# Kernel tuning notes

Hardware: AMD Instinct MI355X
Metric: run time of the kernel (lower is better)

Reference implementation:

```python
import jax, jax.numpy as jnp
import numpy as np

B, N, F = 8, 1024, 256
OUT, REL = 256, 16
NADJ = 7  # ((2 relations + consecutive) * 2 for backward) + self link


def setup_inputs() -> dict:
    key = jax.random.key(0)
    k0, k1, k2, k3, k4 = jax.random.split(key, 5)
    features = jax.random.normal(k0, (B, N, F), dtype=jnp.float32)
    A1 = jax.random.uniform(k1, (B, N, N), dtype=jnp.float32)
    A2 = jax.random.uniform(k2, (B, N, N), dtype=jnp.float32)
    # learned params: one (F+REL, OUT) weight per adjacency matrix, edge embeddings init 'ones', bias (N, OUT)
    W = jax.random.normal(k3, (NADJ, F + REL, OUT), dtype=jnp.float32) * 0.05
    W_edges = jnp.ones((NADJ, REL), dtype=jnp.float32)
    b = jax.random.uniform(k4, (N, OUT), dtype=jnp.float32, minval=-0.05, maxval=0.05)
    return {"features": features, "A1": A1, "A2": A2, "W": W, "W_edges": W_edges, "b": b}


def reference(features, A1, A2, W, W_edges, b):
    # eye = A[0] * zeros(N) + eye(N)  -> batch-broadcast identity [B,N,N]
    eye = jnp.zeros_like(A1) + jnp.eye(N, dtype=A1.dtype)
    # original rolls along axis 0 (batch) of the broadcast identity (faithful replication)
    shifted = jnp.roll(eye, 1, axis=0)
    A_fwd = [A1, A2, shifted]                      # relations + consecutive link
    A_list = A_fwd + [jnp.swapaxes(a, 1, 2) for a in A_fwd]  # backward links
    A_list.append(eye)                             # self links
    A = jnp.stack(A_list, axis=0)                  # [R,B,N,N]

    # concat(features, tile(W_edges[r])) @ W[r] == features @ W[r][:F] + W_edges[r] @ W[r][F:]
    HW = jnp.einsum('bnf,rfo->rbno', features, W[:, :F]) \
         + jnp.einsum('rd,rdo->ro', W_edges, W[:, F:])[:, None, None, :]  # [R,B,N,OUT]
    AHW = jnp.einsum('rbnm,rbmo->rbno', A, HW)     # batched adjacency matmul
    out = jnp.max(AHW, axis=0) + b                 # max-aggregate over relations, add bias
    return out                                     # activation = linear
```

## Files before the change

### kernel.cpp

```cpp
#include <hip/hip_runtime.h>
#include <hip/hip_bf16.h>

#define B_ 8
#define N_ 1024
#define F_ 256
#define OUT_ 256
#define REL_ 16
#define NADJ_ 7

typedef __attribute__((ext_vector_type(8))) _Float16 f16x8;
typedef __attribute__((ext_vector_type(4))) float f32x4;

__device__ __forceinline__ void gll16(const _Float16* g, _Float16* l) {
    __builtin_amdgcn_global_load_lds(
        (const __attribute__((address_space(1))) void*)g,
        (__attribute__((address_space(3))) void*)l, 16, 0, 0);
}

__constant__ const int c_perm[7] = {0, 1, 3, 4, 2, 5, 6};

__global__ __launch_bounds__(256) void prep_kernel(const float* __restrict__ W,
                                                   const float* __restrict__ We,
                                                   const float* __restrict__ feat,
                                                   float* __restrict__ cb,
                                                   _Float16* __restrict__ WTp,
                                                   _Float16* __restrict__ Fe) {
    int bid = blockIdx.x, tid = threadIdx.x;
    if (bid < 7) {
        int idx = bid * 256 + tid;
        int j = idx / OUT_, o = idx % OUT_;
        int r = c_perm[j];
        const float* Wr = W + (size_t)r * (F_ + REL_) * OUT_;
        float s = 0.f;
#pragma unroll
        for (int d = 0; d < REL_; ++d) s += We[r * REL_ + d] * Wr[(F_ + d) * OUT_ + o];
        cb[idx] = s;
    } else if (bid < 1799) {
        int idx = (bid - 7) * 256 + tid;
        int j = idx >> 16, rem = idx & 65535, o = rem >> 8, f = rem & 255;
        int r = c_perm[j];
        WTp[idx] = (_Float16)W[((size_t)r * (F_ + REL_) + f) * OUT_ + o];
    } else {
        int i = (bid - 1799) * 256 + tid;
        size_t base = (size_t)i * 8;
        float4 a = *(const float4*)(feat + base);
        float4 b = *(const float4*)(feat + base + 4);
        f16x8 v = {(_Float16)a.x, (_Float16)a.y, (_Float16)a.z, (_Float16)a.w,
                   (_Float16)b.x, (_Float16)b.y, (_Float16)b.z, (_Float16)b.w};
        *(f16x8*)(Fe + base) = v;
    }
}

__global__ __launch_bounds__(256) void convhw_kernel(const float* __restrict__ A1,
                                                     const float* __restrict__ A2,
                                                     const _Float16* __restrict__ Fe,
                                                     const _Float16* __restrict__ WTp,
                                                     const float* __restrict__ cb,
                                                     _Float16* __restrict__ Af,
                                                     _Float16* __restrict__ HWT,
                                                     _Float16* __restrict__ HWN) {
    __shared__ _Float16 S[8192];
    const int bid = blockIdx.x, tid = threadIdx.x;
    if (bid < 896) {
        const int z = bid / 128, rem = bid % 128, bx = rem & 63, by = rem >> 6;
        const bool tr = (z < 4);
        const _Float16* A  = tr ? (WTp + (size_t)z * 65536) : Fe;
        const _Float16* Bt = tr ? Fe : (WTp + (size_t)z * 65536);
        const int m0 = (tr ? by : bx) * 128;
        const int n0 = (tr ? bx : by) * 128;
        _Float16* As = S;
        _Float16* Bs = S + 4096;
        const int wave = tid >> 6, lane = tid & 63, lm = lane & 15, q = lane >> 4;
        const int wr = (wave >> 1) * 64, wc = (wave & 1) * 64;
        const int srow = tid >> 2, sk = (tid & 3) * 8;
        const _Float16* ga0 = A + (size_t)(m0 + srow) * F_ + sk;
        const _Float16* ga1 = ga0 + (size_t)64 * F_;
        const _Float16* gb0 = Bt + (size_t)(n0 + srow) * F_ + sk;
        const _Float16* gb1 = gb0 + (size_t)64 * F_;
        _Float16* la0 = As + tid * 8;
        _Float16* la1 = As + 2048 + tid * 8;
        _Float16* lb0 = Bs + tid * 8;
        _Float16* lb1 = Bs + 2048 + tid * 8;

        f32x4 acc[4][4] = {};
        for (int k0 = 0; k0 < F_; k0 += 32) {
            gll16(ga0 + k0, la0);
            gll16(ga1 + k0, la1);
            gll16(gb0 + k0, lb0);
            gll16(gb1 + k0, lb1);
            __syncthreads();
            f16x8 af[4], bf[4];
#pragma unroll
            for (int i = 0; i < 4; ++i) af[i] = *(const f16x8*)(As + (wr + i * 16 + lm) * 32 + q * 8);
#pragma unroll
            for (int j = 0; j < 4; ++j) bf[j] = *(const f16x8*)(Bs + (wc + j * 16 + lm) * 32 + q * 8);
#pragma unroll
            for (int i = 0; i < 4; ++i)
#pragma unroll
                for (int j = 0; j < 4; ++j)
                    acc[i][j] = __builtin_amdgcn_mfma_f32_16x16x32_f16(af[i], bf[j], acc[i][j], 0, 0, 0);
            __syncthreads();
        }
        const float* cbz = cb + (size_t)z * 256;
        if (tr) {
            _Float16* C = HWT + (size_t)z * ((size_t)256 * 8192);
#pragma unroll
            for (int i = 0; i < 4; ++i)
#pragma unroll
                for (int j = 0; j < 4; ++j)
#pragma unroll
                    for (int g = 0; g < 4; ++g) {
                        int row = wr + i * 16 + q * 4 + g;
                        int col = wc + j * 16 + lm;
                        float v = acc[i][j][g] + cbz[m0 + row];
                        C[(size_t)(m0 + row) * 8192 + (n0 + col)] = (_Float16)v;
                    }
        } else {
            _Float16* C = HWN + (size_t)(z - 4) * ((size_t)8192 * 256);
#pragma unroll
            for (int i = 0; i < 4; ++i)
#pragma unroll
                for (int j = 0; j < 4; ++j)
#pragma unroll
                    for (int g = 0; g < 4; ++g) {
                        int row = wr + i * 16 + q * 4 + g;
                        int col = wc + j * 16 + lm;
                        float v = acc[i][j][g] + cbz[n0 + col];
                        C[(size_t)(m0 + row) * 256 + (n0 + col)] = (_Float16)v;
                    }
        }
    } else {
        _Float16* T = S;
        const int cbid = bid - 896;
        int z = cbid >> 8, s = z >> 3, b = z & 7;
        const float* src = (s ? A2 : A1) + (size_t)b * N_ * N_;
        int k0 = (cbid & 15) * 64, n0 = ((cbid >> 4) & 15) * 64;
        int r = tid >> 2, cs = (tid & 3) * 16;
        const float* sp = src + (size_t)(k0 + r) * N_ + n0 + cs;
        _Float16 v[16];
#pragma unroll
        for (int j = 0; j < 16; j += 4) {
            float4 f = *(const float4*)(sp + j);
            v[j] = (_Float16)f.x; v[j + 1] = (_Float16)f.y;
            v[j + 2] = (_Float16)f.z; v[j + 3] = (_Float16)f.w;
        }
        const size_t slab = (size_t)8 * N_ * N_;
        {
            _Float16* dst = Af + (size_t)s * slab + (size_t)b * N_ * N_ + (size_t)(k0 + r) * N_ + n0 + cs;
            f16x8 p0 = {v[0], v[1], v[2], v[3], v[4], v[5], v[6], v[7]};
            f16x8 p1 = {v[8], v[9], v[10], v[11], v[12], v[13], v[14], v[15]};
            *(f16x8*)dst = p0;
            *(f16x8*)(dst + 8) = p1;
        }
#pragma unroll
        for (int j = 0; j < 16; ++j) {
            int n = cs + j;
            int sw = ((n ^ (n >> 3)) & 7) << 3;
            T[n * 64 + (r ^ sw)] = v[j];
        }
        __syncthreads();
        {
            int n = tid >> 2, i2 = (tid & 3) * 16;
            int sw = ((n ^ (n >> 3)) & 7) << 3;
            f16x8 q0 = *(const f16x8*)&T[n * 64 + (i2 ^ sw)];
            f16x8 q1 = *(const f16x8*)&T[n * 64 + ((i2 + 8) ^ sw)];
            _Float16* dt = Af + (size_t)(2 + s) * slab + (size_t)b * N_ * N_ + (size_t)(n0 + n) * N_ + k0 + i2;
            *(f16x8*)dt = q0;
            *(f16x8*)(dt + 8) = q1;
        }
    }
}

__global__ __launch_bounds__(256) void p2_kernel(const _Float16* __restrict__ Af,
                                                 const _Float16* __restrict__ HWT,
                                                 _Float16* __restrict__ AHW) {
    __shared__ _Float16 As[128 * 32];
    __shared__ _Float16 Bs[128 * 32];
    const int d = blockIdx.x;
    const int member = (d >> 3) & 1;
    const int p = (d & 7) | ((d >> 4) << 3);
    const int mt = p & 7, zz = p >> 3;
    const int rr = zz >> 3, b = zz & 7;
    const _Float16* A  = Af + (size_t)rr * (8 * 1048576) + (size_t)b * 1048576;
    const _Float16* Bt = HWT + (size_t)rr * (256 * 8192) + (size_t)b * 1024;
    _Float16* C = AHW + (size_t)rr * (8 * 262144) + (size_t)b * 262144;
    const int m0 = mt * 128, n0 = member * 128;
    const int tid = threadIdx.x;
    const int wave = tid >> 6, lane = tid & 63, lm = lane & 15, q = lane >> 4;
    const int wr = (wave >> 1) * 64, wc = (wave & 1) * 64;
    const int srow = tid >> 2, sk = (tid & 3) * 8;
    const _Float16* ga0 = A + (size_t)(m0 + srow) * N_ + sk;
    const _Float16* ga1 = ga0 + (size_t)64 * N_;
    const _Float16* gb0 = Bt + (size_t)(n0 + srow) * 8192 + sk;
    const _Float16* gb1 = gb0 + (size_t)64 * 8192;
    _Float16* la0 = As + tid * 8;
    _Float16* la1 = As + 2048 + tid * 8;
    _Float16* lb0 = Bs + tid * 8;
    _Float16* lb1 = Bs + 2048 + tid * 8;

    f32x4 acc[4][4] = {};
    for (int k0 = 0; k0 < N_; k0 += 32) {
        gll16(ga0 + k0, la0);
        gll16(ga1 + k0, la1);
        gll16(gb0 + k0, lb0);
        gll16(gb1 + k0, lb1);
        __syncthreads();
        f16x8 af[4], bf[4];
#pragma unroll
        for (int i = 0; i < 4; ++i) af[i] = *(const f16x8*)(As + (wr + i * 16 + lm) * 32 + q * 8);
#pragma unroll
        for (int j = 0; j < 4; ++j) bf[j] = *(const f16x8*)(Bs + (wc + j * 16 + lm) * 32 + q * 8);
#pragma unroll
        for (int i = 0; i < 4; ++i)
#pragma unroll
            for (int j = 0; j < 4; ++j)
                acc[i][j] = __builtin_amdgcn_mfma_f32_16x16x32_f16(af[i], bf[j], acc[i][j], 0, 0, 0);
        __syncthreads();
    }
#pragma unroll
    for (int i = 0; i < 4; ++i)
#pragma unroll
        for (int j = 0; j < 4; ++j)
#pragma unroll
            for (int g = 0; g < 4; ++g) {
                int row = wr + i * 16 + q * 4 + g;
                int col = wc + j * 16 + lm;
                C[(size_t)(m0 + row) * 256 + (n0 + col)] = (_Float16)acc[i][j][g];
            }
}

__global__ __launch_bounds__(256) void max_kernel(const _Float16* __restrict__ AHW,
                                                  const _Float16* __restrict__ HWN,
                                                  const float* __restrict__ bias,
                                                  float* __restrict__ out) {
    size_t i = ((size_t)blockIdx.x * 256 + threadIdx.x) * 8;
    const size_t slab = (size_t)B_ * N_ * OUT_;
    float m[8];
    f16x8 v = *(const f16x8*)(AHW + i);
#pragma unroll
    for (int e = 0; e < 8; ++e) m[e] = (float)v[e];
#pragma unroll
    for (int rr = 1; rr < 4; ++rr) {
        f16x8 w = *(const f16x8*)(AHW + rr * slab + i);
#pragma unroll
        for (int e = 0; e < 8; ++e) m[e] = fmaxf(m[e], (float)w[e]);
    }
#pragma unroll
    for (int j = 0; j < 3; ++j) {
        f16x8 w = *(const f16x8*)(HWN + j * slab + i);
#pragma unroll
        for (int e = 0; e < 8; ++e) m[e] = fmaxf(m[e], (float)w[e]);
    }
    size_t bidx = i & ((size_t)N_ * OUT_ - 1);
    float4 b0 = *(const float4*)(bias + bidx);
    float4 b1 = *(const float4*)(bias + bidx + 4);
    float4 o0 = {m[0] + b0.x, m[1] + b0.y, m[2] + b0.z, m[3] + b0.w};
    float4 o1 = {m[4] + b1.x, m[5] + b1.y, m[6] + b1.z, m[7] + b1.w};
    *(float4*)(out + i) = o0;
    *(float4*)(out + i + 4) = o1;
}

__global__ void cbias_kernel(const float* __restrict__ W, const float* __restrict__ We,
                             float* __restrict__ c) {
    int idx = blockIdx.x * 256 + threadIdx.x;
    if (idx >= NADJ_ * OUT_) return;
    int r = idx / OUT_, o = idx % OUT_;
    const float* Wr = W + (size_t)r * (F_ + REL_) * OUT_;
    float s = 0.f;
#pragma unroll
    for (int d = 0; d < REL_; ++d) s += We[r * REL_ + d] * Wr[(F_ + d) * OUT_ + o];
    c[idx] = s;
}

__global__ __launch_bounds__(256) void hw_kernel(const float* __restrict__ feat,
                                                 const float* __restrict__ W,
                                                 const float* __restrict__ cb,
                                                 _Float16* __restrict__ HWb) {
    __shared__ _Float16 As[64][32];
    __shared__ _Float16 Bs[64][32];
    const int mt = blockIdx.x, ct = blockIdx.y;
    const int tid = threadIdx.x, wave = tid >> 6, lane = tid & 63;
    const int r = (ct * 64) / OUT_;
    const int o0 = (ct * 64) % OUT_;
    const float* Bg = W + (size_t)r * (F_ + REL_) * OUT_ + o0;
    const int m0 = mt * 64;
    const int lm = lane & 15, q = lane >> 4;
    f32x4 acc[4] = {};
    for (int k0 = 0; k0 < F_; k0 += 32) {
        {
            int seg = (tid & 3) * 8, m = tid >> 2;
            const float* src = feat + (size_t)(m0 + m) * F_ + k0 + seg;
#pragma unroll
            for (int j = 0; j < 8; ++j) As[m][seg + j] = (_Float16)src[j];
        }
        {
            int kk = tid >> 3, ns = (tid & 7) * 8;
            const float* src = Bg + (size_t)(k0 + kk) * OUT_ + ns;
#pragma unroll
            for (int j = 0; j < 8; ++j) Bs[ns + j][kk] = (_Float16)src[j];
        }
        __syncthreads();
        f16x8 a = *(const f16x8*)&As[wave * 16 + lm][q * 8];
#pragma unroll
        for (int c4 = 0; c4 < 4; ++c4) {
            f16x8 b = *(const f16x8*)&Bs[c4 * 16 + lm][q * 8];
            acc[c4] = __builtin_amdgcn_mfma_f32_16x16x32_f16(a, b, acc[c4], 0, 0, 0);
        }
        __syncthreads();
    }
#pragma unroll
    for (int c4 = 0; c4 < 4; ++c4)
#pragma unroll
        for (int g = 0; g < 4; ++g) {
            int row = wave * 16 + (lane >> 4) * 4 + g;
            int col = c4 * 16 + lm;
            float v = acc[c4][g] + cb[r * OUT_ + o0 + col];
            HWb[((size_t)r * B_ * N_ + m0 + row) * OUT_ + o0 + col] = (_Float16)v;
        }
}

__global__ __launch_bounds__(256) void agg_kernel(const float* __restrict__ A1,
                                                  const float* __restrict__ A2,
                                                  const _Float16* __restrict__ HWb,
                                                  const float* __restrict__ bias,
                                                  float* __restrict__ out) {
    __shared__ _Float16 As[64][32];
    __shared__ _Float16 Bs[64][32];
    const int b = blockIdx.z, nt = blockIdx.y, ot = blockIdx.x;
    const int tid = threadIdx.x, wave = tid >> 6, lane = tid & 63;
    const int n0 = nt * 64, o0 = ot * 64;
    const int lm = lane & 15, q = lane >> 4;
    const size_t rstride = (size_t)B_ * N_ * OUT_;
    f32x4 mx[4];
#pragma unroll
    for (int i = 0; i < 4; ++i) mx[i] = f32x4{-1e30f, -1e30f, -1e30f, -1e30f};
#pragma unroll 1
    for (int rr = 0; rr < 4; ++rr) {
        const float* Ag = ((rr & 1) ? A2 : A1) + (size_t)b * N_ * N_;
        const bool tr = (rr >= 2);
        const int r = (rr < 2) ? rr : rr + 1;
        const _Float16* Bg = HWb + (size_t)r * rstride + (size_t)b * N_ * OUT_ + o0;
        f32x4 acc[4] = {};
        for (int k0 = 0; k0 < N_; k0 += 32) {
            if (!tr) {
                int seg = (tid & 3) * 8, m = tid >> 2;
                const float* src = Ag + (size_t)(n0 + m) * N_ + k0 + seg;
#pragma unroll
                for (int j = 0; j < 8; ++j) As[m][seg + j] = (_Float16)src[j];
            } else {
                int kk = tid >> 3, ms = (tid & 7) * 8;
                const float* src = Ag + (size_t)(k0 + kk) * N_ + n0 + ms;
#pragma unroll
                for (int j = 0; j < 8; ++j) As[ms + j][kk] = (_Float16)src[j];
            }
            {
                int kk = tid >> 3, ns = (tid & 7) * 8;
                const _Float16* src = Bg + (size_t)(k0 + kk) * OUT_ + ns;
#pragma unroll
                for (int j = 0; j < 8; ++j) Bs[ns + j][kk] = src[j];
            }
            __syncthreads();
            f16x8 a = *(const f16x8*)&As[wave * 16 + lm][q * 8];
#pragma unroll
            for (int c4 = 0; c4 < 4; ++c4) {
                f16x8 bb = *(const f16x8*)&Bs[c4 * 16 + lm][q * 8];
                acc[c4] = __builtin_amdgcn_mfma_f32_16x16x32_f16(a, bb, acc[c4], 0, 0, 0);
            }
            __syncthreads();
        }
#pragma unroll
        for (int c4 = 0; c4 < 4; ++c4)
#pragma unroll
            for (int g = 0; g < 4; ++g) mx[c4][g] = fmaxf(mx[c4][g], acc[c4][g]);
    }
#pragma unroll
    for (int c4 = 0; c4 < 4; ++c4)
#pragma unroll
        for (int g = 0; g < 4; ++g) {
            int row = wave * 16 + (lane >> 4) * 4 + g;
            int col = c4 * 16 + lm;
            size_t pos = ((size_t)b * N_ + n0 + row) * OUT_ + o0 + col;
            float v = mx[c4][g];
            v = fmaxf(v, (float)HWb[2 * rstride + pos]);
            v = fmaxf(v, (float)HWb[5 * rstride + pos]);
            v = fmaxf(v, (float)HWb[6 * rstride + pos]);
            out[pos] = v + bias[((size_t)(n0 + row)) * OUT_ + o0 + col];
        }
}

extern "C" void kernel_launch(void* const* d_in, const int* in_sizes, int n_in,
                              void* d_out, int out_size, void* d_ws, size_t ws_size,
                              hipStream_t stream) {
    const float* feat = (const float*)d_in[0];
    const float* A1   = (const float*)d_in[1];
    const float* A2   = (const float*)d_in[2];
    const float* W    = (const float*)d_in[3];
    const float* We   = (const float*)d_in[4];
    const float* bias = (const float*)d_in[5];
    float* out = (float*)d_out;

    const size_t OFF_CB   = 0;
    const size_t OFF_WT   = 8192;
    const size_t OFF_FE   = 1048576;
    const size_t OFF_AF   = 5242880;
    const size_t OFF_HWT  = 72351744;
    const size_t OFF_HWN  = 89128960;
    const size_t OFF_AHW  = 101711872;
    const size_t WS_NEEDED = 118489088;

    if (ws_size >= WS_NEEDED) {
        float*    cbp = (float*)((char*)d_ws + OFF_CB);
        _Float16* WTp = (_Float16*)((char*)d_ws + OFF_WT);
        _Float16* Fe  = (_Float16*)((char*)d_ws + OFF_FE);
        _Float16* Af  = (_Float16*)((char*)d_ws + OFF_AF);
        _Float16* HWT = (_Float16*)((char*)d_ws + OFF_HWT);
        _Float16* HWN = (_Float16*)((char*)d_ws + OFF_HWN);
        _Float16* AHW = (_Float16*)((char*)d_ws + OFF_AHW);

        prep_kernel<<<2823, 256, 0, stream>>>(W, We, feat, cbp, WTp, Fe);
        convhw_kernel<<<4992, 256, 0, stream>>>(A1, A2, Fe, WTp, cbp, Af, HWT, HWN);
        p2_kernel<<<512, 256, 0, stream>>>(Af, HWT, AHW);
        max_kernel<<<1024, 256, 0, stream>>>(AHW, HWN, bias, out);
    } else {
        float* cb = (float*)d_ws;
        _Float16* HWb = (_Float16*)((char*)d_ws + 8192);
        cbias_kernel<<<7, 256, 0, stream>>>(W, We, cb);
        hw_kernel<<<dim3(128, 28), 256, 0, stream>>>(feat, W, cb, HWb);
        agg_kernel<<<dim3(4, 16, 8), 256, 0, stream>>>(A1, A2, HWb, bias, out);
    }
}
```

Before: 176.7 us.

## Fuse fp32-to-fp16 conversion of forward adjacency into GEMM A-tile loads

The conversion kernel no longer writes an fp16 copy of the untransposed A1/A2; it only writes the transposed copies, now at slab indices 0 and 1. For the two forward relations, the GEMM kernel reads fp32 A1/A2 directly, converts to fp16 in registers, prefetches the next K-slice, and stores to LDS. This removes one fp16 write pass plus its later reread, at the cost of reading twice as many bytes for the A tiles in the GEMM. The register-staged path also replaces the async global-to-LDS loads for these blocks.

```diff
diff --git a/kernel.cpp b/kernel.cpp
--- a/kernel.cpp
+++ b/kernel.cpp
@@ -145,13 +145,6 @@
             v[j + 2] = (_Float16)f.z; v[j + 3] = (_Float16)f.w;
         }
         const size_t slab = (size_t)8 * N_ * N_;
-        {
-            _Float16* dst = Af + (size_t)s * slab + (size_t)b * N_ * N_ + (size_t)(k0 + r) * N_ + n0 + cs;
-            f16x8 p0 = {v[0], v[1], v[2], v[3], v[4], v[5], v[6], v[7]};
-            f16x8 p1 = {v[8], v[9], v[10], v[11], v[12], v[13], v[14], v[15]};
-            *(f16x8*)dst = p0;
-            *(f16x8*)(dst + 8) = p1;
-        }
 #pragma unroll
         for (int j = 0; j < 16; ++j) {
             int n = cs + j;
@@ -164,14 +157,16 @@
             int sw = ((n ^ (n >> 3)) & 7) << 3;
             f16x8 q0 = *(const f16x8*)&T[n * 64 + (i2 ^ sw)];
             f16x8 q1 = *(const f16x8*)&T[n * 64 + ((i2 + 8) ^ sw)];
-            _Float16* dt = Af + (size_t)(2 + s) * slab + (size_t)b * N_ * N_ + (size_t)(n0 + n) * N_ + k0 + i2;
+            _Float16* dt = Af + (size_t)s * slab + (size_t)b * N_ * N_ + (size_t)(n0 + n) * N_ + k0 + i2;
             *(f16x8*)dt = q0;
             *(f16x8*)(dt + 8) = q1;
         }
     }
 }
 
-__global__ __launch_bounds__(256) void p2_kernel(const _Float16* __restrict__ Af,
+__global__ __launch_bounds__(256) void p2_kernel(const float* __restrict__ A1,
+                                                 const float* __restrict__ A2,
+                                                 const _Float16* __restrict__ Af,
                                                  const _Float16* __restrict__ HWT,
                                                  _Float16* __restrict__ AHW) {
     __shared__ _Float16 As[128 * 32];
@@ -181,7 +176,6 @@
     const int p = (d & 7) | ((d >> 4) << 3);
     const int mt = p & 7, zz = p >> 3;
     const int rr = zz >> 3, b = zz & 7;
-    const _Float16* A  = Af + (size_t)rr * (8 * 1048576) + (size_t)b * 1048576;
     const _Float16* Bt = HWT + (size_t)rr * (256 * 8192) + (size_t)b * 1024;
     _Float16* C = AHW + (size_t)rr * (8 * 262144) + (size_t)b * 262144;
     const int m0 = mt * 128, n0 = member * 128;
@@ -189,8 +183,6 @@
     const int wave = tid >> 6, lane = tid & 63, lm = lane & 15, q = lane >> 4;
     const int wr = (wave >> 1) * 64, wc = (wave & 1) * 64;
     const int srow = tid >> 2, sk = (tid & 3) * 8;
-    const _Float16* ga0 = A + (size_t)(m0 + srow) * N_ + sk;
-    const _Float16* ga1 = ga0 + (size_t)64 * N_;
     const _Float16* gb0 = Bt + (size_t)(n0 + srow) * 8192 + sk;
     const _Float16* gb1 = gb0 + (size_t)64 * 8192;
     _Float16* la0 = As + tid * 8;
@@ -199,23 +191,64 @@
     _Float16* lb1 = Bs + 2048 + tid * 8;
 
     f32x4 acc[4][4] = {};
-    for (int k0 = 0; k0 < N_; k0 += 32) {
-        gll16(ga0 + k0, la0);
-        gll16(ga1 + k0, la1);
-        gll16(gb0 + k0, lb0);
-        gll16(gb1 + k0, lb1);
-        __syncthreads();
-        f16x8 af[4], bf[4];
-#pragma unroll
-        for (int i = 0; i < 4; ++i) af[i] = *(const f16x8*)(As + (wr + i * 16 + lm) * 32 + q * 8);
-#pragma unroll
-        for (int j = 0; j < 4; ++j) bf[j] = *(const f16x8*)(Bs + (wc + j * 16 + lm) * 32 + q * 8);
-#pragma unroll
-        for (int i = 0; i < 4; ++i)
-#pragma unroll
-            for (int j = 0; j < 4; ++j)
-                acc[i][j] = __builtin_amdgcn_mfma_f32_16x16x32_f16(af[i], bf[j], acc[i][j], 0, 0, 0);
-        __syncthreads();
+    if (rr < 2) {
+        const float* Ag0 = ((rr & 1) ? A2 : A1) + (size_t)b * N_ * N_
+                           + (size_t)(m0 + srow) * N_ + sk;
+        const float* Ag1 = Ag0 + (size_t)64 * N_;
+        float4 pa0 = *(const float4*)(Ag0);
+        float4 pa1 = *(const float4*)(Ag0 + 4);
+        float4 pb0 = *(const float4*)(Ag1);
+        float4 pb1 = *(const float4*)(Ag1 + 4);
+        for (int k0 = 0; k0 < N_; k0 += 32) {
+            f16x8 v0 = {(_Float16)pa0.x, (_Float16)pa0.y, (_Float16)pa0.z, (_Float16)pa0.w,
+                        (_Float16)pa1.x, (_Float16)pa1.y, (_Float16)pa1.z, (_Float16)pa1.w};
+            f16x8 v1 = {(_Float16)pb0.x, (_Float16)pb0.y, (_Float16)pb0.z, (_Float16)pb0.w,
+                        (_Float16)pb1.x, (_Float16)pb1.y, (_Float16)pb1.z, (_Float16)pb1.w};
+            *(f16x8*)la0 = v0;
+            *(f16x8*)la1 = v1;
+            gll16(gb0 + k0, lb0);
+            gll16(gb1 + k0, lb1);
+            if (k0 + 32 < N_) {
+                pa0 = *(const float4*)(Ag0 + k0 + 32);
+                pa1 = *(const float4*)(Ag0 + k0 + 36);
+                pb0 = *(const float4*)(Ag1 + k0 + 32);
+                pb1 = *(const float4*)(Ag1 + k0 + 36);
+            }
+            __syncthreads();
+            f16x8 af[4], bf[4];
+#pragma unroll
+            for (int i = 0; i < 4; ++i) af[i] = *(const f16x8*)(As + (wr + i * 16 + lm) * 32 + q * 8);
+#pragma unroll
+            for (int j = 0; j < 4; ++j) bf[j] = *(const f16x8*)(Bs + (wc + j * 16 + lm) * 32 + q * 8);
+#pragma unroll
+            for (int i = 0; i < 4; ++i)
+#pragma unroll
+                for (int j = 0; j < 4; ++j)
+                    acc[i][j] = __builtin_amdgcn_mfma_f32_16x16x32_f16(af[i], bf[j], acc[i][j], 0, 0, 0);
+            __syncthreads();
+        }
+    } else {
+        const _Float16* ga0 = Af + (size_t)(rr - 2) * (8 * 1048576) + (size_t)b * 1048576
+                              + (size_t)(m0 + srow) * N_ + sk;
+        const _Float16* ga1 = ga0 + (size_t)64 * N_;
+        for (int k0 = 0; k0 < N_; k0 += 32) {
+            gll16(ga0 + k0, la0);
+            gll16(ga1 + k0, la1);
+            gll16(gb0 + k0, lb0);
+            gll16(gb1 + k0, lb1);
+            __syncthreads();
+            f16x8 af[4], bf[4];
+#pragma unroll
+            for (int i = 0; i < 4; ++i) af[i] = *(const f16x8*)(As + (wr + i * 16 + lm) * 32 + q * 8);
+#pragma unroll
+            for (int j = 0; j < 4; ++j) bf[j] = *(const f16x8*)(Bs + (wc + j * 16 + lm) * 32 + q * 8);
+#pragma unroll
+            for (int i = 0; i < 4; ++i)
+#pragma unroll
+                for (int j = 0; j < 4; ++j)
+                    acc[i][j] = __builtin_amdgcn_mfma_f32_16x16x32_f16(af[i], bf[j], acc[i][j], 0, 0, 0);
+            __syncthreads();
+        }
     }
 #pragma unroll
     for (int i = 0; i < 4; ++i)
@@ -419,7 +452,7 @@
 
         prep_kernel<<<2823, 256, 0, stream>>>(W, We, feat, cbp, WTp, Fe);
         convhw_kernel<<<4992, 256, 0, stream>>>(A1, A2, Fe, WTp, cbp, Af, HWT, HWN);
-        p2_kernel<<<512, 256, 0, stream>>>(Af, HWT, AHW);
+        p2_kernel<<<512, 256, 0, stream>>>(A1, A2, Af, HWT, AHW);
         max_kernel<<<1024, 256, 0, stream>>>(AHW, HWN, bias, out);
     } else {
         float* cb = (float*)d_ws;
```

Result: no change. 176.4 us (-0.2%).
